# Kernel optimization log

Hardware: AMD Instinct MI355X
Metric: run time of the kernel (lower is better)

The kernel has to match this reference:

```python
import jax, jax.numpy as jnp
import numpy as np

HEADS = 8
EPS = 1e-5


def _quad_sums(a):
    """a: (B,h,H,W,...) -> (B,h,H,W,4,...) sums over the four inclusive
    quadrants [ :h+1,:w+1 | :h+1,w: | h:,:w+1 | h:,w: ] for every (h,w),
    via padded 2D prefix sums over axes (2,3)."""
    c = jnp.cumsum(jnp.cumsum(a, axis=2), axis=3)
    pads = [(0, 0)] * a.ndim
    pads[2] = (1, 0)
    pads[3] = (1, 0)
    P = jnp.pad(c, pads)  # P[...,i,j,...] = sum over rows<i, cols<j
    tl = P[:, :, 1:, 1:]
    tr = P[:, :, 1:, -1:] - P[:, :, 1:, :-1]
    bl = P[:, :, -1:, 1:] - P[:, :, :-1, 1:]
    br = P[:, :, -1:, -1:] - P[:, :, :-1, -1:] - P[:, :, -1:, :-1] + P[:, :, :-1, :-1]
    return jnp.stack([tl, tr, bl, br], axis=4)


def setup_inputs():
    key = jax.random.key(0)
    ks = jax.random.split(key, 12)
    B, H, W, D = 64, 48, 48, 64
    n = H * W
    hD = HEADS * D  # inner_dim = heads * dim_head, dim_head == dim
    rn = lambda k, shape: jax.random.normal(k, shape, dtype=jnp.float32) * 0.02
    return {
        "x": jax.random.normal(ks[0], (B, n, D), dtype=jnp.float32),
        "ln_g": jnp.ones((D,), jnp.float32),
        "ln_b": jnp.zeros((D,), jnp.float32),
        "Wqkv": rn(ks[1], (3 * hD, D)),
        "bqkv": jnp.zeros((3 * hD,), jnp.float32),
        "cls_tok": rn(ks[2], (D,)),
        "Wwqkv": rn(ks[3], (3 * D, D)),
        "bwqkv": jnp.zeros((3 * D,), jnp.float32),
        "Wwproj": rn(ks[4], (D, D)),
        "bwproj": jnp.zeros((D,), jnp.float32),
        "Wraq": rn(ks[5], (D, D)),
        "Wrak": rn(ks[6], (D, D)),
        "Wrav": rn(ks[7], (D, D)),
        "Wrao": rn(ks[8], (D, D)),
        "brao": jnp.zeros((D,), jnp.float32),
        "Wout": rn(ks[9], (D, hD)),
        "bout": jnp.zeros((D,), jnp.float32),
    }


def reference(x, ln_g, ln_b, Wqkv, bqkv, cls_tok, Wwqkv, bwqkv, Wwproj, bwproj,
              Wraq, Wrak, Wrav, Wrao, brao, Wout, bout):
    B, n, D = x.shape
    H = W = int(np.sqrt(n))
    h = HEADS
    hd = D // h                      # WindowAttention head dim
    scale_w = hd ** -0.5             # WindowAttention qk scale
    scale_ra = (D // h) ** -0.5      # RegionAggregator scale

    # LayerNorm (biased variance, as torch)
    mu = x.mean(-1, keepdims=True)
    var = ((x - mu) ** 2).mean(-1, keepdims=True)
    xn = (x - mu) / jnp.sqrt(var + EPS) * ln_g + ln_b

    # to_qkv: only q is consumed downstream (k, v are dead in the original forward)
    q = xn @ Wqkv[: h * D].T + bqkv[: h * D]
    q = q.reshape(B, n, h, D).transpose(0, 2, 1, 3)  # (B,h,n,D)  d == dim

    # WindowAttention: per-quadrant CLS-row attention, shared token keys/values.
    cls_qkv = (cls_tok @ Wwqkv.T + bwqkv).reshape(3, h, hd)
    q_c = cls_qkv[0] * scale_w                       # (h,hd) scaled cls query
    k_c, v_c = cls_qkv[1], cls_qkv[2]
    tok = (xn @ Wwqkv.T + bwqkv).reshape(B, n, 3, h, hd)
    k_t = tok[:, :, 1].transpose(0, 2, 1, 3)         # (B,h,n,hd)
    v_t = tok[:, :, 2].transpose(0, 2, 1, 3)
    logits = jnp.einsum('hd,bhnd->bhn', q_c, k_t)    # cls -> token logits
    cls_logit = jnp.einsum('hd,hd->h', q_c, k_c)     # cls -> cls logit
    m = jnp.maximum(logits.max(-1), cls_logit)       # (B,h) stabilizer
    e = jnp.exp(logits - m[..., None]).reshape(B, h, H, W)
    ecls = jnp.exp(cls_logit - m)                    # (B,h)
    ev = e[..., None] * v_t.reshape(B, h, H, W, hd)
    Se = _quad_sums(e)                               # (B,h,H,W,4)
    Sev = _quad_sums(ev)                             # (B,h,H,W,4,hd)
    denom = ecls[:, :, None, None, None] + Se
    num = ecls[:, :, None, None, None, None] * v_c[None, :, None, None, None, :] + Sev
    cls_out = num / denom[..., None]                 # (B,h,H,W,4,hd)
    cls_out = cls_out.transpose(0, 2, 3, 4, 1, 5).reshape(B, n, 4, D)
    regions = cls_out @ Wwproj.T + bwproj            # (B,n,4,D)

    # RegionAggregator (regions are identical across heads -> broadcast)
    qp = jnp.einsum('bhnd,ed->bhne', q, Wraq)
    kp = regions @ Wrak.T                            # (B,n,4,D)
    vp = regions @ Wrav.T
    scores = jnp.einsum('bhnd,bnrd->bhnr', qp, kp) * scale_ra
    attn = jax.nn.softmax(scores, axis=-1)
    agg = jnp.einsum('bhnr,bnrd->bhnd', attn, vp)
    out = agg @ Wrao.T + brao                        # (B,h,n,D)
    out = out.transpose(0, 2, 1, 3).reshape(B, n, h * D)
    return out @ Wout.T + bout                       # (B,n,D)
```

## Files before the change

kernel.cpp:

```cpp
#include <hip/hip_runtime.h>
#include <math.h>


#define SCALE_W  0.3535533905932738f
#define SCALE_RA 0.3535533905932738f
#define LN_EPS 1e-5f

typedef __attribute__((ext_vector_type(8))) short bf16x8;
typedef __attribute__((ext_vector_type(4))) float f32x4;

#define OFF_XN   0ull
#define SZ_XN    (64ull*2304*64)
#define OFF_KT   (OFF_XN + SZ_XN)
#define SZ_KT    (64ull*8*2304*8)
#define OFF_VT   (OFF_KT + SZ_KT)
#define OFF_PA   (OFF_VT + SZ_KT)
#define SZ_PA    (512ull*2401*5)
#define OFF_PB   (OFF_PA + SZ_PA)
#define SZ_PB    (512ull*2401*4)
#define OFF_ECLS (OFF_PB + SZ_PB)
#define OFF_QC   (OFF_ECLS + 512)
#define OFF_KC   (OFF_QC + 64)
#define OFF_VC   (OFF_KC + 64)
#define OFF_CLOG (OFF_VC + 64)
#define OFF_BK   (OFF_CLOG + 8)
#define OFF_BV   (OFF_BK + 64)
#define OFF_AH   (OFF_BV + 64)
#define OFF_W1   (OFF_AH + 512)
#define OFF_WZ   (OFF_W1 + 64)
#define OFF_B2   (OFF_WZ + 64)
#define OFF_V2   (OFF_B2 + 512)
#define OFF_UH   (OFF_V2 + 512)
#define OFF_CH   (OFF_UH + 512)
#define OFF_C1   (OFF_CH + 8)
#define OFF_G    (OFF_C1 + 64)
#define OFF_Z    (OFF_G + 32768)

__device__ inline void split2(float x, unsigned short &h, unsigned short &l) {
  unsigned u = __float_as_uint(x);
  unsigned hr = (u + 0x7fffu + ((u >> 16) & 1u)) >> 16;
  h = (unsigned short)hr;
  float hf = __uint_as_float(hr << 16);
  float lo = x - hf;
  unsigned u2 = __float_as_uint(lo);
  l = (unsigned short)((u2 + 0x7fffu + ((u2 >> 16) & 1u)) >> 16);
}

__device__ inline void split2x2(float x0, float x1, unsigned &h, unsigned &l) {
  asm("v_cvt_pk_bf16_f32 %0, %1, %2" : "=v"(h) : "v"(x0), "v"(x1));
  float r0 = x0 - __uint_as_float(h << 16);
  float r1 = x1 - __uint_as_float(h & 0xffff0000u);
  asm("v_cvt_pk_bf16_f32 %0, %1, %2" : "=v"(l) : "v"(r0), "v"(r1));
}

__device__ inline float dot64(const float* __restrict__ a, const float* __restrict__ b) {
  float s0 = 0.f, s1 = 0.f, s2 = 0.f, s3 = 0.f;
  #pragma unroll
  for (int d = 0; d < 64; d += 4) {
    float4 av = *(const float4*)(a + d);
    float4 bv = *(const float4*)(b + d);
    s0 += av.x * bv.x; s1 += av.y * bv.y;
    s2 += av.z * bv.z; s3 += av.w * bv.w;
  }
  return (s0 + s1) + (s2 + s3);
}

__global__ void k_setup1(const float* __restrict__ Wqkv, const float* __restrict__ bqkv,
                         const float* __restrict__ cls_tok, const float* __restrict__ Wwqkv,
                         const float* __restrict__ bwqkv, const float* __restrict__ Wwproj,
                         const float* __restrict__ bwproj, const float* __restrict__ Wraq,
                         const float* __restrict__ Wrak, const float* __restrict__ Wrav,
                         const float* __restrict__ Wrao, const float* __restrict__ brao,
                         const float* __restrict__ Wout, const float* __restrict__ bout,
                         float* __restrict__ ws) {
  __shared__ float bwz[64];
  int tid = threadIdx.x;
  for (int idx = tid; idx < 768; idx += 256) {
    if (idx < 192) {
      float s = bwqkv[idx] + dot64(Wwqkv + idx*64, cls_tok);
      if (idx < 64) ws[OFF_QC + idx] = s * SCALE_W;
      else if (idx < 128) ws[OFF_KC + idx - 64] = s;
      else ws[OFF_VC + idx - 128] = s;
    } else if (idx < 256) {
      int e = idx - 192;
      ws[OFF_BV + e] = dot64(Wrav + e*64, bwproj);
    } else {
      int t2 = idx - 256; int hh = t2 >> 6, e = t2 & 63;
      ws[OFF_AH + t2] = dot64(Wraq + e*64, bqkv + hh*64);
    }
  }
  __syncthreads();
  for (int idx = tid; idx < 584; idx += 256) {
    if (idx < 8) {
      float s = 0.f;
      for (int u = 0; u < 8; ++u) s += ws[OFF_QC + idx*8+u] * ws[OFF_KC + idx*8+u];
      ws[OFF_CLOG + idx] = s;
    } else if (idx < 72) {
      int e = idx - 8;
      ws[OFF_WZ + e] = dot64(Wrao + e*64, ws + OFF_BV);
    } else {
      int t2 = idx - 72; int hh = t2 >> 6, e = t2 & 63; float s = 0.f;
      for (int d = 0; d < 64; ++d) s += Wrak[d*64+e] * ws[OFF_AH + hh*64+d];
      ws[OFF_B2 + t2] = s;
    }
  }
  __syncthreads();
  if (tid < 64) bwz[tid] = brao[tid] + ws[OFF_WZ + tid];
  __syncthreads();
  for (int idx = tid; idx < 576; idx += 256) {
    if (idx < 512) {
      int hh = idx >> 6, e = idx & 63; float s = 0.f;
      for (int d = 0; d < 64; ++d) s += Wwproj[d*64+e] * ws[OFF_B2 + hh*64+d];
      ws[OFF_V2 + idx] = s;
    } else {
      int e = idx - 512;
      float s0 = 0.f, s1 = 0.f, s2 = 0.f, s3 = 0.f;
      for (int f = 0; f < 512; f += 4) {
        float4 w4 = *(const float4*)(Wout + e*512 + f);
        float4 b4 = *(const float4*)&bwz[f & 63];
        s0 += w4.x*b4.x; s1 += w4.y*b4.y; s2 += w4.z*b4.z; s3 += w4.w*b4.w;
      }
      ws[OFF_C1 + e] = bout[e] + (s0 + s1) + (s2 + s3);
    }
  }
}

__global__ __launch_bounds__(256) void k_setupW(const float* __restrict__ Wqkv,
      const float* __restrict__ Wraq, const float* __restrict__ Wrak,
      const float* __restrict__ Wrav, const float* __restrict__ Wrao,
      const float* __restrict__ Wwproj, const float* __restrict__ Wout,
      float* __restrict__ ws) {
  __shared__ float A[64*65];
  __shared__ float Bl[64*65];
  int tid = threadIdx.x;
  int blk = blockIdx.x;
  if (blk < 8) {
    int hh = blk;
    for (int o = tid; o < 4096; o += 256) {
      int d = o & 63, e = o >> 6; float s = 0.f;
      for (int f = 0; f < 64; ++f) s += Wraq[f*64+d] * Wrak[f*64+e];
      A[d*65 + e] = s;
    }
    __syncthreads();
    for (int o = tid; o < 4096; o += 256) {
      int j = o & 63, i = o >> 6; float s = 0.f;
      for (int f = 0; f < 64; ++f) s += A[i*65 + f] * Wwproj[f*64 + j];
      Bl[i*65 + j] = s;
    }
    __syncthreads();
    unsigned short* gb = (unsigned short*)(ws + OFF_G) + hh*8192;
    for (int o = tid; o < 4096; o += 256) {
      int d = o & 63, e = o >> 6; float s = 0.f;
      for (int f = 0; f < 64; ++f) s += Wqkv[(hh*64+f)*64 + d] * Bl[f*65 + e];
      unsigned short h16, l16;
      split2(s, h16, l16);
      int base = (e >> 4)*2048 + (d >> 5)*1024 + (((d >> 3) & 3)*16 + (e & 15))*8 + (d & 7);
      gb[base]       = h16;
      gb[base + 512] = l16;
    }
  } else {
    int hh = blk - 8;
    for (int o = tid; o < 4096; o += 256) {
      int d = o & 63, e = o >> 6; float s = 0.f;
      for (int f = 0; f < 64; ++f) s += Wrav[e*64+f] * Wwproj[f*64+d];
      A[e*65 + d] = s;
    }
    __syncthreads();
    for (int o = tid; o < 4096; o += 256) {
      int d = o & 63, i = o >> 6; float s = 0.f;
      for (int f = 0; f < 64; ++f) s += Wrao[i*64+f] * A[f*65 + d];
      Bl[i*65 + d] = s;
    }
    __syncthreads();
    unsigned short* zb = (unsigned short*)(ws + OFF_Z) + hh*8192;
    for (int o = tid; o < 4096; o += 256) {
      int d = o & 63, e = o >> 6; float s = 0.f;
      for (int f = 0; f < 64; ++f) s += Wout[e*512 + hh*64 + f] * Bl[f*65 + d];
      unsigned short h16, l16;
      split2(s, h16, l16);
      int base = (e >> 4)*2048 + (d >> 5)*1024 + (((d >> 3) & 3)*16 + (e & 15))*8 + (d & 7);
      zb[base]       = h16;
      zb[base + 512] = l16;
    }
  }
}

__global__ __launch_bounds__(256) void k_lnkv(const float* __restrict__ x,
      const float* __restrict__ ln_g, const float* __restrict__ ln_b,
      const float* __restrict__ Wwqkv, const float* __restrict__ bwqkv,
      float* __restrict__ ws) {
  __shared__ float sm[4352 + 8448 + 128];
  float* xnT = sm;
  float* xt  = sm + 4352;
  float* wkv = sm + 4352;
  float* muL = sm + 4352 + 8448;
  float* rsL = muL + 64;

  int tid = threadIdx.x;
  long T0 = (long)blockIdx.x * 64;
  int tok = tid >> 2, seg = tid & 3;

  const float4* x4 = (const float4*)(x + (T0 + tok)*64 + seg*16);
  float4 va = x4[0], vb = x4[1], vc4 = x4[2], vd = x4[3];
  {
    float* xp = xt + tok*65 + seg*16;
    xp[0]=va.x; xp[1]=va.y; xp[2]=va.z; xp[3]=va.w;
    xp[4]=vb.x; xp[5]=vb.y; xp[6]=vb.z; xp[7]=vb.w;
    xp[8]=vc4.x; xp[9]=vc4.y; xp[10]=vc4.z; xp[11]=vc4.w;
    xp[12]=vd.x; xp[13]=vd.y; xp[14]=vd.z; xp[15]=vd.w;
  }
  __syncthreads();
  if (tid < 64) {
    float s = 0.f;
    for (int i2 = 0; i2 < 64; ++i2) s += xt[tid*65 + i2];
    float mu = s * (1.0f/64.0f);
    float v = 0.f;
    for (int i2 = 0; i2 < 64; ++i2) { float d = xt[tid*65 + i2] - mu; v += d*d; }
    v *= (1.0f/64.0f);
    muL[tid] = mu; rsL[tid] = 1.0f / sqrtf(v + LN_EPS);
  }
  __syncthreads();
  {
    float mu = muL[tok], rs = rsL[tok];
    float xv[16];
    #pragma unroll
    for (int k = 0; k < 16; ++k) {
      int i2 = seg*16 + k;
      float v = (xt[tok*65 + i2] - mu) * rs * ln_g[i2] + ln_b[i2];
      xv[k] = v;
      xnT[i2*68 + tok] = v;
    }
    float4* xng = (float4*)(ws + OFF_XN + (T0 + tok)*64 + seg*16);
    xng[0] = make_float4(xv[0], xv[1], xv[2], xv[3]);
    xng[1] = make_float4(xv[4], xv[5], xv[6], xv[7]);
    xng[2] = make_float4(xv[8], xv[9], xv[10], xv[11]);
    xng[3] = make_float4(xv[12], xv[13], xv[14], xv[15]);
  }
  __syncthreads();
  {
    int o = tid >> 1, dh = (tid & 1) * 32;
    #pragma unroll
    for (int k = 0; k < 32; k += 4) {
      float4 w4 = *(const float4*)(Wwqkv + (64 + o)*64 + dh + k);
      wkv[(dh+k+0)*132 + o] = w4.x;
      wkv[(dh+k+1)*132 + o] = w4.y;
      wkv[(dh+k+2)*132 + o] = w4.z;
      wkv[(dh+k+3)*132 + o] = w4.w;
    }
  }
  __syncthreads();
  int tokq = tid & 15, og = tid >> 4;
  float acc[4][8];
  #pragma unroll
  for (int ti = 0; ti < 4; ++ti)
    #pragma unroll
    for (int k = 0; k < 8; ++k) acc[ti][k] = 0.f;
  for (int d2 = 0; d2 < 64; ++d2) {
    float4 a4 = *(float4*)&xnT[d2*68 + tokq*4];
    float4 b0 = *(float4*)&wkv[d2*132 + og*8];
    float4 b1 = *(float4*)&wkv[d2*132 + og*8 + 4];
    float aa[4] = {a4.x, a4.y, a4.z, a4.w};
    float bbv[8] = {b0.x,b0.y,b0.z,b0.w,b1.x,b1.y,b1.z,b1.w};
    #pragma unroll
    for (int ti = 0; ti < 4; ++ti)
      #pragma unroll
      for (int k = 0; k < 8; ++k) acc[ti][k] += aa[ti]*bbv[k];
  }
  int hh2 = og & 7;
  float bsv[8];
  #pragma unroll
  for (int k = 0; k < 8; ++k) bsv[k] = bwqkv[64 + og*8 + k];
  unsigned long long dstoff = (og < 8) ? OFF_KT : OFF_VT;
  #pragma unroll
  for (int ti = 0; ti < 4; ++ti) {
    long ntok = T0 + tokq*4 + ti;
    int bb = (int)(ntok / 2304);
    int nl = (int)(ntok % 2304);
    float* dst = ws + dstoff + ((long)(bb*8 + hh2)*2304 + nl)*8;
    *(float4*)dst = make_float4(acc[ti][0]+bsv[0], acc[ti][1]+bsv[1], acc[ti][2]+bsv[2], acc[ti][3]+bsv[3]);
    *(float4*)(dst+4) = make_float4(acc[ti][4]+bsv[4], acc[ti][5]+bsv[5], acc[ti][6]+bsv[6], acc[ti][7]+bsv[7]);
  }
}

__global__ __launch_bounds__(256) void k_prefix(float* __restrict__ ws) {
  __shared__ float Pp[49*49*5];
  __shared__ float red[4];
  int tid = threadIdx.x;
  int blk = blockIdx.x;
  int g = blk & 1, bh = blk >> 1;
  int hh = bh & 7;
  const float* kt = ws + OFF_KT + (long)bh*2304*8;
  const float* vt = ws + OFF_VT + (long)bh*2304*8 + (g ? 4 : 0);
  float qc[8];
  #pragma unroll
  for (int u = 0; u < 8; ++u) qc[u] = ws[OFF_QC + hh*8 + u];
  float lgr[9];
  float mloc = -1e30f;
  #pragma unroll
  for (int it = 0; it < 9; ++it) {
    int nn = tid + it*256;
    const float4* kk = (const float4*)(kt + nn*8);
    float4 k0 = kk[0], k1 = kk[1];
    float lv = qc[0]*k0.x + qc[1]*k0.y + qc[2]*k0.z + qc[3]*k0.w
             + qc[4]*k1.x + qc[5]*k1.y + qc[6]*k1.z + qc[7]*k1.w;
    lgr[it] = lv;
    mloc = fmaxf(mloc, lv);
  }
  #pragma unroll
  for (int mk = 1; mk < 64; mk <<= 1) mloc = fmaxf(mloc, __shfl_xor(mloc, mk, 64));
  if ((tid & 63) == 0) red[tid >> 6] = mloc;
  __syncthreads();
  float m = fmaxf(fmaxf(red[0], red[1]), fmaxf(red[2], red[3]));
  m = fmaxf(m, ws[OFF_CLOG + hh]);
  if (tid == 0 && g == 0) ws[OFF_ECLS + bh] = __expf(ws[OFF_CLOG + hh] - m);
  #pragma unroll
  for (int it = 0; it < 9; ++it) {
    int nn = tid + it*256;
    int i2 = nn / 48, j2 = nn % 48;
    float ev = __expf(lgr[it] - m);
    float4 v4 = *(const float4*)(vt + nn*8);
    float* cell = &Pp[((i2+1)*49 + (j2+1))*5];
    if (g == 0) {
      cell[0] = ev; cell[1] = ev*v4.x; cell[2] = ev*v4.y; cell[3] = ev*v4.z; cell[4] = ev*v4.w;
    } else {
      cell[0] = ev*v4.x; cell[1] = ev*v4.y; cell[2] = ev*v4.z; cell[3] = ev*v4.w;
    }
  }
  __syncthreads();
  int nc = g ? 4 : 5;
  for (int idx = tid; idx < 48*nc; idx += 256) {
    int j2 = idx / nc + 1, c = idx % nc;
    float s = 0.f;
    for (int i0 = 1; i0 <= 48; i0 += 8) {
      float v[8];
      #pragma unroll
      for (int k = 0; k < 8; ++k) v[k] = Pp[((i0+k)*49 + j2)*5 + c];
      #pragma unroll
      for (int k = 0; k < 8; ++k) { s += v[k]; v[k] = s; }
      #pragma unroll
      for (int k = 0; k < 8; ++k) Pp[((i0+k)*49 + j2)*5 + c] = v[k];
    }
  }
  __syncthreads();
  for (int idx = tid; idx < 48*nc; idx += 256) {
    int i2 = idx / nc + 1, c = idx % nc;
    float s = 0.f;
    for (int j0 = 1; j0 <= 48; j0 += 8) {
      float v[8];
      #pragma unroll
      for (int k = 0; k < 8; ++k) v[k] = Pp[(i2*49 + j0+k)*5 + c];
      #pragma unroll
      for (int k = 0; k < 8; ++k) { s += v[k]; v[k] = s; }
      #pragma unroll
      for (int k = 0; k < 8; ++k) Pp[(i2*49 + j0+k)*5 + c] = v[k];
    }
  }
  __syncthreads();
  if (g == 0) {
    float* pa = ws + OFF_PA + (long)bh*12005;
    for (int idx = tid; idx < 12005; idx += 256) {
      int cell = idx / 5;
      int ii = cell / 49, jj = cell % 49;
      pa[idx] = (ii && jj) ? Pp[idx] : 0.f;
    }
  } else {
    float* pb = ws + OFF_PB + (long)bh*9604;
    for (int idx = tid; idx < 9604; idx += 256) {
      int cell = idx >> 2, c = idx & 3;
      int ii = cell / 49, jj = cell % 49;
      pb[idx] = (ii && jj) ? Pp[cell*5 + c] : 0.f;
    }
  }
}

__global__ __launch_bounds__(128) void k_main(const float* __restrict__ ws,
                                              float* __restrict__ outp) {
  __shared__ __align__(16) unsigned short XNhi[16*64];
  __shared__ __align__(16) unsigned short XNlo[16*64];
  __shared__ __align__(16) unsigned short CBhi[16*128];
  __shared__ __align__(16) unsigned short CBlo[16*128];
  __shared__ __align__(16) float Tlds[16*128];

  int tid = threadIdx.x;
  int tok = tid >> 3, eg = tid & 7;
  int lane = tid & 63, wv = tid >> 6;
  int quad = lane >> 4, lrow = lane & 15;
  int wcol = wv;
  long T0 = (long)blockIdx.x * 16;
  int b = (int)(T0 / 2304);
  int n = (int)(T0 % 2304) + tok;
  int i2 = n / 48, j2 = n % 48;

  {
    const float4* p4 = (const float4*)(ws + OFF_XN + (T0 + tok)*64 + eg*8);
    float4 xa = p4[0], xb = p4[1];
    float xv[8] = {xa.x, xa.y, xa.z, xa.w, xb.x, xb.y, xb.z, xb.w};
    union { unsigned u[4]; uint2 d[2]; } ph, pl;
    #pragma unroll
    for (int k = 0; k < 8; k += 2) split2x2(xv[k], xv[k+1], ph.u[k>>1], pl.u[k>>1]);
    int off = tok*64 + ((eg*8) ^ ((tok & 7) << 3));
    *(uint2*)&XNhi[off]     = ph.d[0];
    *(uint2*)&XNhi[off + 4] = ph.d[1];
    *(uint2*)&XNlo[off]     = pl.d[0];
    *(uint2*)&XNlo[off + 4] = pl.d[1];
  }

  float cls0[8], cls1[8], cls2[8], cls3[8];
  {
    float ec = ws[OFF_ECLS + b*8 + eg];
    const float* PA = ws + OFF_PA + (long)(b*8 + eg)*12005;
    const float* PB = ws + OFF_PB + (long)(b*8 + eg)*9604;
    int c_ij  = i2*49 + j2;
    int c_ij1 = c_ij + 1;
    int c_iW  = i2*49 + 48;
    int c_1j  = c_ij + 49;
    int c_1j1 = c_1j + 1;
    int c_1W  = c_iW + 49;
    int c_Hj  = 48*49 + j2;
    int c_Hj1 = c_Hj + 1;
    int c_HW  = 48*49 + 48;
    float rden[4];
    {
      float tl = PA[c_1j1*5];
      float tr = PA[c_1W*5] - PA[c_1j*5];
      float bl = PA[c_Hj1*5] - PA[c_ij1*5];
      float br = PA[c_HW*5] - PA[c_iW*5] - PA[c_Hj*5] + PA[c_ij*5];
      rden[0] = 1.0f/(ec + tl); rden[1] = 1.0f/(ec + tr);
      rden[2] = 1.0f/(ec + bl); rden[3] = 1.0f/(ec + br);
    }
    #pragma unroll
    for (int u = 0; u < 4; ++u) {
      int c = 1 + u;
      float tl = PA[c_1j1*5 + c];
      float tr = PA[c_1W*5 + c] - PA[c_1j*5 + c];
      float bl = PA[c_Hj1*5 + c] - PA[c_ij1*5 + c];
      float br = PA[c_HW*5 + c] - PA[c_iW*5 + c] - PA[c_Hj*5 + c] + PA[c_ij*5 + c];
      float nv = ec * ws[OFF_VC + eg*8 + u];
      cls0[u] = (nv + tl) * rden[0];
      cls1[u] = (nv + tr) * rden[1];
      cls2[u] = (nv + bl) * rden[2];
      cls3[u] = (nv + br) * rden[3];
    }
    #pragma unroll
    for (int u = 4; u < 8; ++u) {
      int c = u - 4;
      float tl = PB[c_1j1*4 + c];
      float tr = PB[c_1W*4 + c] - PB[c_1j*4 + c];
      float bl = PB[c_Hj1*4 + c] - PB[c_ij1*4 + c];
      float br = PB[c_HW*4 + c] - PB[c_iW*4 + c] - PB[c_Hj*4 + c] + PB[c_ij*4 + c];
      float nv = ec * ws[OFF_VC + eg*8 + u];
      cls0[u] = (nv + tl) * rden[0];
      cls1[u] = (nv + tr) * rden[1];
      cls2[u] = (nv + bl) * rden[2];
      cls3[u] = (nv + br) * rden[3];
    }
  }
  __syncthreads();

  const unsigned short* gball = (const unsigned short*)(ws + OFF_G);
  const unsigned short* zball = (const unsigned short*)(ws + OFF_Z);

  f32x4 oa0 = {0.f,0.f,0.f,0.f};
  f32x4 oa1 = {0.f,0.f,0.f,0.f};

  int rr = lrow;
  int sw3 = (rr & 7) << 3;
  const unsigned short* arh = XNhi + rr*64;
  const unsigned short* arl = XNlo + rr*64;
  const unsigned short* crh = CBhi + rr*128;
  const unsigned short* crl = CBlo + rr*128;

  for (int it = 0; it < 4; ++it) {
    int h0 = it*2;
    {
      union { bf16x8 v; uint2 d[2]; } ah0, ah1, al0, al1;
      int oa = (quad*8) ^ sw3;
      int ob = (32 + quad*8) ^ sw3;
      ah0.d[0] = *(const uint2*)(arh + oa); ah0.d[1] = *(const uint2*)(arh + oa + 4);
      ah1.d[0] = *(const uint2*)(arh + ob); ah1.d[1] = *(const uint2*)(arh + ob + 4);
      al0.d[0] = *(const uint2*)(arl + oa); al0.d[1] = *(const uint2*)(arl + oa + 4);
      al1.d[0] = *(const uint2*)(arl + ob); al1.d[1] = *(const uint2*)(arl + ob + 4);
      #pragma unroll
      for (int c = 0; c < 4; ++c) {
        int colb = wcol*4 + c;
        int e0 = colb*16 + lrow;
        const unsigned short* gh = gball + (h0 + (colb >> 2))*8192 + (colb & 3)*2048 + lane*8;
        bf16x8 bh0 = *(const bf16x8*)(gh);
        bf16x8 bl0 = *(const bf16x8*)(gh + 512);
        bf16x8 bh1 = *(const bf16x8*)(gh + 1024);
        bf16x8 bl1 = *(const bf16x8*)(gh + 1536);
        f32x4 acc = {0.f,0.f,0.f,0.f};
        acc = __builtin_amdgcn_mfma_f32_16x16x32_bf16(ah0.v, bh0, acc, 0, 0, 0);
        acc = __builtin_amdgcn_mfma_f32_16x16x32_bf16(ah1.v, bh1, acc, 0, 0, 0);
        acc = __builtin_amdgcn_mfma_f32_16x16x32_bf16(al0.v, bh0, acc, 0, 0, 0);
        acc = __builtin_amdgcn_mfma_f32_16x16x32_bf16(al1.v, bh1, acc, 0, 0, 0);
        acc = __builtin_amdgcn_mfma_f32_16x16x32_bf16(ah0.v, bl0, acc, 0, 0, 0);
        acc = __builtin_amdgcn_mfma_f32_16x16x32_bf16(ah1.v, bl1, acc, 0, 0, 0);
        float v2v = ws[OFF_V2 + h0*64 + e0];
        #pragma unroll
        for (int r = 0; r < 4; ++r) {
          int trow = quad*4 + r;
          Tlds[trow*128 + (e0 ^ ((trow & 7) << 2))] = acc[r] + v2v;
        }
      }
    }
    __syncthreads();
    {
      float tv0[8], tv1[8];
      {
        int base = tok*128;
        int sw2 = (tok & 7) << 2;
        float4 a0 = *(const float4*)&Tlds[base + ((eg*8) ^ sw2)];
        float4 b0 = *(const float4*)&Tlds[base + ((eg*8 + 4) ^ sw2)];
        float4 a1 = *(const float4*)&Tlds[base + ((64 + eg*8) ^ sw2)];
        float4 b1 = *(const float4*)&Tlds[base + ((64 + eg*8 + 4) ^ sw2)];
        tv0[0]=a0.x; tv0[1]=a0.y; tv0[2]=a0.z; tv0[3]=a0.w;
        tv0[4]=b0.x; tv0[5]=b0.y; tv0[6]=b0.z; tv0[7]=b0.w;
        tv1[0]=a1.x; tv1[1]=a1.y; tv1[2]=a1.z; tv1[3]=a1.w;
        tv1[4]=b1.x; tv1[5]=b1.y; tv1[6]=b1.z; tv1[7]=b1.w;
      }
      float p0=0.f,p1=0.f,p2=0.f,p3=0.f,q0=0.f,q1=0.f,q2=0.f,q3=0.f;
      #pragma unroll
      for (int k = 0; k < 8; ++k) {
        p0 += tv0[k]*cls0[k]; p1 += tv0[k]*cls1[k];
        p2 += tv0[k]*cls2[k]; p3 += tv0[k]*cls3[k];
        q0 += tv1[k]*cls0[k]; q1 += tv1[k]*cls1[k];
        q2 += tv1[k]*cls2[k]; q3 += tv1[k]*cls3[k];
      }
      #pragma unroll
      for (int mk = 1; mk < 8; mk <<= 1) {
        p0 += __shfl_xor(p0, mk, 8); p1 += __shfl_xor(p1, mk, 8);
        p2 += __shfl_xor(p2, mk, 8); p3 += __shfl_xor(p3, mk, 8);
        q0 += __shfl_xor(q0, mk, 8); q1 += __shfl_xor(q1, mk, 8);
        q2 += __shfl_xor(q2, mk, 8); q3 += __shfl_xor(q3, mk, 8);
      }
      union { unsigned u[4]; uint2 d[2]; } ch, cl;
      int cbBase = tok*128;
      int swc = (tok & 7) << 3;
      {
        float s0 = p0*SCALE_RA, s1 = p1*SCALE_RA, s2 = p2*SCALE_RA, s3 = p3*SCALE_RA;
        float mm = fmaxf(fmaxf(s0, s1), fmaxf(s2, s3));
        float e0 = __expf(s0-mm), e1 = __expf(s1-mm), e2 = __expf(s2-mm), e3 = __expf(s3-mm);
        float inv = 1.0f/(e0+e1+e2+e3);
        float av0 = e0*inv, av1 = e1*inv, av2 = e2*inv, av3 = e3*inv;
        #pragma unroll
        for (int k = 0; k < 8; k += 2) {
          float cv0 = av0*cls0[k] + av1*cls1[k] + av2*cls2[k] + av3*cls3[k];
          float cv1 = av0*cls0[k+1] + av1*cls1[k+1] + av2*cls2[k+1] + av3*cls3[k+1];
          split2x2(cv0, cv1, ch.u[k>>1], cl.u[k>>1]);
        }
        int o = cbBase + ((eg*8) ^ swc);
        *(uint2*)&CBhi[o]     = ch.d[0]; *(uint2*)&CBhi[o + 4] = ch.d[1];
        *(uint2*)&CBlo[o]     = cl.d[0]; *(uint2*)&CBlo[o + 4] = cl.d[1];
      }
      {
        float s0 = q0*SCALE_RA, s1 = q1*SCALE_RA, s2 = q2*SCALE_RA, s3 = q3*SCALE_RA;
        float mm = fmaxf(fmaxf(s0, s1), fmaxf(s2, s3));
        float e0 = __expf(s0-mm), e1 = __expf(s1-mm), e2 = __expf(s2-mm), e3 = __expf(s3-mm);
        float inv = 1.0f/(e0+e1+e2+e3);
        float av0 = e0*inv, av1 = e1*inv, av2 = e2*inv, av3 = e3*inv;
        #pragma unroll
        for (int k = 0; k < 8; k += 2) {
          float cv0 = av0*cls0[k] + av1*cls1[k] + av2*cls2[k] + av3*cls3[k];
          float cv1 = av0*cls0[k+1] + av1*cls1[k+1] + av2*cls2[k+1] + av3*cls3[k+1];
          split2x2(cv0, cv1, ch.u[k>>1], cl.u[k>>1]);
        }
        int o = cbBase + ((64 + eg*8) ^ swc);
        *(uint2*)&CBhi[o]     = ch.d[0]; *(uint2*)&CBhi[o + 4] = ch.d[1];
        *(uint2*)&CBlo[o]     = cl.d[0]; *(uint2*)&CBlo[o + 4] = cl.d[1];
      }
    }
    __syncthreads();
    {
      #pragma unroll
      for (int c = 0; c < 2; ++c) {
        int colb = wcol*2 + c;
        int e0 = colb*16 + lrow;
        f32x4 acc = (c == 0) ? oa0 : oa1;
        #pragma unroll
        for (int kb = 0; kb < 4; ++kb) {
          union { bf16x8 v; uint2 d[2]; } ah, al;
          int o = (kb*32 + quad*8) ^ sw3;
          ah.d[0] = *(const uint2*)(crh + o); ah.d[1] = *(const uint2*)(crh + o + 4);
          al.d[0] = *(const uint2*)(crl + o); al.d[1] = *(const uint2*)(crl + o + 4);
          const unsigned short* zc = zball + (h0 + (kb >> 1))*8192 + colb*2048 + (kb & 1)*1024 + lane*8;
          bf16x8 bh = *(const bf16x8*)(zc);
          bf16x8 bl = *(const bf16x8*)(zc + 512);
          acc = __builtin_amdgcn_mfma_f32_16x16x32_bf16(ah.v, bh, acc, 0, 0, 0);
          acc = __builtin_amdgcn_mfma_f32_16x16x32_bf16(al.v, bh, acc, 0, 0, 0);
          acc = __builtin_amdgcn_mfma_f32_16x16x32_bf16(ah.v, bl, acc, 0, 0, 0);
        }
        if (c == 0) oa0 = acc; else oa1 = acc;
      }
    }
  }
  #pragma unroll
  for (int c = 0; c < 2; ++c) {
    int e0 = (wcol*2 + c)*16 + lrow;
    float cov = ws[OFF_C1 + e0];
    f32x4 oa = (c == 0) ? oa0 : oa1;
    #pragma unroll
    for (int r = 0; r < 4; ++r)
      outp[(T0 + quad*4 + r)*64 + e0] = oa[r] + cov;
  }
}

extern "C" void kernel_launch(void* const* d_in, const int* in_sizes, int n_in,
                              void* d_out, int out_size, void* d_ws, size_t ws_size,
                              hipStream_t stream) {
  const float* x      = (const float*)d_in[0];
  const float* ln_g   = (const float*)d_in[1];
  const float* ln_b   = (const float*)d_in[2];
  const float* Wqkv   = (const float*)d_in[3];
  const float* bqkv   = (const float*)d_in[4];
  const float* cls_tok= (const float*)d_in[5];
  const float* Wwqkv  = (const float*)d_in[6];
  const float* bwqkv  = (const float*)d_in[7];
  const float* Wwproj = (const float*)d_in[8];
  const float* bwproj = (const float*)d_in[9];
  const float* Wraq   = (const float*)d_in[10];
  const float* Wrak   = (const float*)d_in[11];
  const float* Wrav   = (const float*)d_in[12];
  const float* Wrao   = (const float*)d_in[13];
  const float* brao   = (const float*)d_in[14];
  const float* Wout   = (const float*)d_in[15];
  const float* bout   = (const float*)d_in[16];
  float* ws = (float*)d_ws;
  float* outp = (float*)d_out;

  hipLaunchKernelGGL(k_setup1, dim3(1), dim3(256), 0, stream,
                     Wqkv, bqkv, cls_tok, Wwqkv, bwqkv, Wwproj, bwproj,
                     Wraq, Wrak, Wrav, Wrao, brao, Wout, bout, ws);
  hipLaunchKernelGGL(k_setupW, dim3(16), dim3(256), 0, stream,
                     Wqkv, Wraq, Wrak, Wrav, Wrao, Wwproj, Wout, ws);
  hipLaunchKernelGGL(k_lnkv, dim3(2304), dim3(256), 0, stream, x, ln_g, ln_b, Wwqkv, bwqkv, ws);
  hipLaunchKernelGGL(k_prefix, dim3(1024), dim3(256), 0, stream, ws);
  hipLaunchKernelGGL(k_main, dim3(9216), dim3(128), 0, stream, ws, outp);
}
```

Baseline: 404.7 us.

## Merge setup and layernorm kernels into one launch, widen prefix blocks

Three preprocessing kernels (scalar setup, weight folding, layernorm+KV projection) are merged into a single kernel that picks its role by block index, removing two launches and the serialization between the small setup kernels and the large LN kernel. The prefix-sum kernel moves from 256 to 512 threads, so each thread does fewer tokens and the column/row scans run in one pass. In the main kernel the A-fragment LDS loads are hoisted out of the head loop. The setup blocks now run alongside LN blocks, and their long serial tail can extend the fused kernel.

```diff
diff --git a/kernel.cpp b/kernel.cpp
--- a/kernel.cpp
+++ b/kernel.cpp
@@ -65,226 +65,219 @@
   return (s0 + s1) + (s2 + s3);
 }
 
-__global__ void k_setup1(const float* __restrict__ Wqkv, const float* __restrict__ bqkv,
-                         const float* __restrict__ cls_tok, const float* __restrict__ Wwqkv,
-                         const float* __restrict__ bwqkv, const float* __restrict__ Wwproj,
-                         const float* __restrict__ bwproj, const float* __restrict__ Wraq,
-                         const float* __restrict__ Wrak, const float* __restrict__ Wrav,
-                         const float* __restrict__ Wrao, const float* __restrict__ brao,
-                         const float* __restrict__ Wout, const float* __restrict__ bout,
-                         float* __restrict__ ws) {
-  __shared__ float bwz[64];
-  int tid = threadIdx.x;
-  for (int idx = tid; idx < 768; idx += 256) {
-    if (idx < 192) {
-      float s = bwqkv[idx] + dot64(Wwqkv + idx*64, cls_tok);
-      if (idx < 64) ws[OFF_QC + idx] = s * SCALE_W;
-      else if (idx < 128) ws[OFF_KC + idx - 64] = s;
-      else ws[OFF_VC + idx - 128] = s;
-    } else if (idx < 256) {
-      int e = idx - 192;
-      ws[OFF_BV + e] = dot64(Wrav + e*64, bwproj);
-    } else {
-      int t2 = idx - 256; int hh = t2 >> 6, e = t2 & 63;
-      ws[OFF_AH + t2] = dot64(Wraq + e*64, bqkv + hh*64);
-    }
-  }
-  __syncthreads();
-  for (int idx = tid; idx < 584; idx += 256) {
-    if (idx < 8) {
-      float s = 0.f;
-      for (int u = 0; u < 8; ++u) s += ws[OFF_QC + idx*8+u] * ws[OFF_KC + idx*8+u];
-      ws[OFF_CLOG + idx] = s;
-    } else if (idx < 72) {
-      int e = idx - 8;
-      ws[OFF_WZ + e] = dot64(Wrao + e*64, ws + OFF_BV);
-    } else {
-      int t2 = idx - 72; int hh = t2 >> 6, e = t2 & 63; float s = 0.f;
-      for (int d = 0; d < 64; ++d) s += Wrak[d*64+e] * ws[OFF_AH + hh*64+d];
-      ws[OFF_B2 + t2] = s;
-    }
-  }
-  __syncthreads();
-  if (tid < 64) bwz[tid] = brao[tid] + ws[OFF_WZ + tid];
-  __syncthreads();
-  for (int idx = tid; idx < 576; idx += 256) {
-    if (idx < 512) {
-      int hh = idx >> 6, e = idx & 63; float s = 0.f;
-      for (int d = 0; d < 64; ++d) s += Wwproj[d*64+e] * ws[OFF_B2 + hh*64+d];
-      ws[OFF_V2 + idx] = s;
-    } else {
-      int e = idx - 512;
-      float s0 = 0.f, s1 = 0.f, s2 = 0.f, s3 = 0.f;
-      for (int f = 0; f < 512; f += 4) {
-        float4 w4 = *(const float4*)(Wout + e*512 + f);
-        float4 b4 = *(const float4*)&bwz[f & 63];
-        s0 += w4.x*b4.x; s1 += w4.y*b4.y; s2 += w4.z*b4.z; s3 += w4.w*b4.w;
-      }
-      ws[OFF_C1 + e] = bout[e] + (s0 + s1) + (s2 + s3);
-    }
-  }
-}
-
-__global__ __launch_bounds__(256) void k_setupW(const float* __restrict__ Wqkv,
-      const float* __restrict__ Wraq, const float* __restrict__ Wrak,
-      const float* __restrict__ Wrav, const float* __restrict__ Wrao,
-      const float* __restrict__ Wwproj, const float* __restrict__ Wout,
+__global__ __launch_bounds__(256) void k_pre(const float* __restrict__ x,
+      const float* __restrict__ ln_g, const float* __restrict__ ln_b,
+      const float* __restrict__ Wqkv, const float* __restrict__ bqkv,
+      const float* __restrict__ cls_tok, const float* __restrict__ Wwqkv,
+      const float* __restrict__ bwqkv, const float* __restrict__ Wwproj,
+      const float* __restrict__ bwproj, const float* __restrict__ Wraq,
+      const float* __restrict__ Wrak, const float* __restrict__ Wrav,
+      const float* __restrict__ Wrao, const float* __restrict__ brao,
+      const float* __restrict__ Wout, const float* __restrict__ bout,
       float* __restrict__ ws) {
-  __shared__ float A[64*65];
-  __shared__ float Bl[64*65];
+  __shared__ float smu[12928];
   int tid = threadIdx.x;
   int blk = blockIdx.x;
-  if (blk < 8) {
-    int hh = blk;
-    for (int o = tid; o < 4096; o += 256) {
-      int d = o & 63, e = o >> 6; float s = 0.f;
-      for (int f = 0; f < 64; ++f) s += Wraq[f*64+d] * Wrak[f*64+e];
-      A[d*65 + e] = s;
-    }
-    __syncthreads();
-    for (int o = tid; o < 4096; o += 256) {
-      int j = o & 63, i = o >> 6; float s = 0.f;
-      for (int f = 0; f < 64; ++f) s += A[i*65 + f] * Wwproj[f*64 + j];
-      Bl[i*65 + j] = s;
-    }
-    __syncthreads();
-    unsigned short* gb = (unsigned short*)(ws + OFF_G) + hh*8192;
-    for (int o = tid; o < 4096; o += 256) {
-      int d = o & 63, e = o >> 6; float s = 0.f;
-      for (int f = 0; f < 64; ++f) s += Wqkv[(hh*64+f)*64 + d] * Bl[f*65 + e];
-      unsigned short h16, l16;
-      split2(s, h16, l16);
-      int base = (e >> 4)*2048 + (d >> 5)*1024 + (((d >> 3) & 3)*16 + (e & 15))*8 + (d & 7);
-      gb[base]       = h16;
-      gb[base + 512] = l16;
-    }
-  } else {
-    int hh = blk - 8;
-    for (int o = tid; o < 4096; o += 256) {
-      int d = o & 63, e = o >> 6; float s = 0.f;
-      for (int f = 0; f < 64; ++f) s += Wrav[e*64+f] * Wwproj[f*64+d];
-      A[e*65 + d] = s;
-    }
-    __syncthreads();
-    for (int o = tid; o < 4096; o += 256) {
-      int d = o & 63, i = o >> 6; float s = 0.f;
-      for (int f = 0; f < 64; ++f) s += Wrao[i*64+f] * A[f*65 + d];
-      Bl[i*65 + d] = s;
-    }
-    __syncthreads();
-    unsigned short* zb = (unsigned short*)(ws + OFF_Z) + hh*8192;
-    for (int o = tid; o < 4096; o += 256) {
-      int d = o & 63, e = o >> 6; float s = 0.f;
-      for (int f = 0; f < 64; ++f) s += Wout[e*512 + hh*64 + f] * Bl[f*65 + d];
-      unsigned short h16, l16;
-      split2(s, h16, l16);
-      int base = (e >> 4)*2048 + (d >> 5)*1024 + (((d >> 3) & 3)*16 + (e & 15))*8 + (d & 7);
-      zb[base]       = h16;
-      zb[base + 512] = l16;
-    }
-  }
-}
-
-__global__ __launch_bounds__(256) void k_lnkv(const float* __restrict__ x,
-      const float* __restrict__ ln_g, const float* __restrict__ ln_b,
-      const float* __restrict__ Wwqkv, const float* __restrict__ bwqkv,
-      float* __restrict__ ws) {
-  __shared__ float sm[4352 + 8448 + 128];
-  float* xnT = sm;
-  float* xt  = sm + 4352;
-  float* wkv = sm + 4352;
-  float* muL = sm + 4352 + 8448;
-  float* rsL = muL + 64;
-
-  int tid = threadIdx.x;
-  long T0 = (long)blockIdx.x * 64;
-  int tok = tid >> 2, seg = tid & 3;
-
-  const float4* x4 = (const float4*)(x + (T0 + tok)*64 + seg*16);
-  float4 va = x4[0], vb = x4[1], vc4 = x4[2], vd = x4[3];
-  {
-    float* xp = xt + tok*65 + seg*16;
-    xp[0]=va.x; xp[1]=va.y; xp[2]=va.z; xp[3]=va.w;
-    xp[4]=vb.x; xp[5]=vb.y; xp[6]=vb.z; xp[7]=vb.w;
-    xp[8]=vc4.x; xp[9]=vc4.y; xp[10]=vc4.z; xp[11]=vc4.w;
-    xp[12]=vd.x; xp[13]=vd.y; xp[14]=vd.z; xp[15]=vd.w;
-  }
-  __syncthreads();
-  if (tid < 64) {
-    float s = 0.f;
-    for (int i2 = 0; i2 < 64; ++i2) s += xt[tid*65 + i2];
-    float mu = s * (1.0f/64.0f);
-    float v = 0.f;
-    for (int i2 = 0; i2 < 64; ++i2) { float d = xt[tid*65 + i2] - mu; v += d*d; }
-    v *= (1.0f/64.0f);
-    muL[tid] = mu; rsL[tid] = 1.0f / sqrtf(v + LN_EPS);
-  }
-  __syncthreads();
-  {
-    float mu = muL[tok], rs = rsL[tok];
-    float xv[16];
-    #pragma unroll
-    for (int k = 0; k < 16; ++k) {
-      int i2 = seg*16 + k;
-      float v = (xt[tok*65 + i2] - mu) * rs * ln_g[i2] + ln_b[i2];
-      xv[k] = v;
-      xnT[i2*68 + tok] = v;
-    }
-    float4* xng = (float4*)(ws + OFF_XN + (T0 + tok)*64 + seg*16);
-    xng[0] = make_float4(xv[0], xv[1], xv[2], xv[3]);
-    xng[1] = make_float4(xv[4], xv[5], xv[6], xv[7]);
-    xng[2] = make_float4(xv[8], xv[9], xv[10], xv[11]);
-    xng[3] = make_float4(xv[12], xv[13], xv[14], xv[15]);
-  }
-  __syncthreads();
-  {
-    int o = tid >> 1, dh = (tid & 1) * 32;
-    #pragma unroll
-    for (int k = 0; k < 32; k += 4) {
-      float4 w4 = *(const float4*)(Wwqkv + (64 + o)*64 + dh + k);
-      wkv[(dh+k+0)*132 + o] = w4.x;
-      wkv[(dh+k+1)*132 + o] = w4.y;
-      wkv[(dh+k+2)*132 + o] = w4.z;
-      wkv[(dh+k+3)*132 + o] = w4.w;
-    }
-  }
-  __syncthreads();
-  int tokq = tid & 15, og = tid >> 4;
-  float acc[4][8];
-  #pragma unroll
-  for (int ti = 0; ti < 4; ++ti)
-    #pragma unroll
-    for (int k = 0; k < 8; ++k) acc[ti][k] = 0.f;
-  for (int d2 = 0; d2 < 64; ++d2) {
-    float4 a4 = *(float4*)&xnT[d2*68 + tokq*4];
-    float4 b0 = *(float4*)&wkv[d2*132 + og*8];
-    float4 b1 = *(float4*)&wkv[d2*132 + og*8 + 4];
-    float aa[4] = {a4.x, a4.y, a4.z, a4.w};
-    float bbv[8] = {b0.x,b0.y,b0.z,b0.w,b1.x,b1.y,b1.z,b1.w};
+
+  if (blk < 2304) {
+    float* xnT = smu;
+    float* xt  = smu + 4352;
+    float* wkv = smu + 4352;
+    float* muL = smu + 4352 + 8448;
+    float* rsL = muL + 64;
+
+    long T0 = (long)blk * 64;
+    int tok = tid >> 2, seg = tid & 3;
+
+    const float4* x4 = (const float4*)(x + (T0 + tok)*64 + seg*16);
+    float4 va = x4[0], vb = x4[1], vc4 = x4[2], vd = x4[3];
+    {
+      float* xp = xt + tok*65 + seg*16;
+      xp[0]=va.x; xp[1]=va.y; xp[2]=va.z; xp[3]=va.w;
+      xp[4]=vb.x; xp[5]=vb.y; xp[6]=vb.z; xp[7]=vb.w;
+      xp[8]=vc4.x; xp[9]=vc4.y; xp[10]=vc4.z; xp[11]=vc4.w;
+      xp[12]=vd.x; xp[13]=vd.y; xp[14]=vd.z; xp[15]=vd.w;
+    }
+    __syncthreads();
+    if (tid < 64) {
+      float s = 0.f;
+      for (int i2 = 0; i2 < 64; ++i2) s += xt[tid*65 + i2];
+      float mu = s * (1.0f/64.0f);
+      float v = 0.f;
+      for (int i2 = 0; i2 < 64; ++i2) { float d = xt[tid*65 + i2] - mu; v += d*d; }
+      v *= (1.0f/64.0f);
+      muL[tid] = mu; rsL[tid] = 1.0f / sqrtf(v + LN_EPS);
+    }
+    __syncthreads();
+    {
+      float mu = muL[tok], rs = rsL[tok];
+      float xv[16];
+      #pragma unroll
+      for (int k = 0; k < 16; ++k) {
+        int i2 = seg*16 + k;
+        float v = (xt[tok*65 + i2] - mu) * rs * ln_g[i2] + ln_b[i2];
+        xv[k] = v;
+        xnT[i2*68 + tok] = v;
+      }
+      float4* xng = (float4*)(ws + OFF_XN + (T0 + tok)*64 + seg*16);
+      xng[0] = make_float4(xv[0], xv[1], xv[2], xv[3]);
+      xng[1] = make_float4(xv[4], xv[5], xv[6], xv[7]);
+      xng[2] = make_float4(xv[8], xv[9], xv[10], xv[11]);
+      xng[3] = make_float4(xv[12], xv[13], xv[14], xv[15]);
+    }
+    __syncthreads();
+    {
+      int o = tid >> 1, dh = (tid & 1) * 32;
+      #pragma unroll
+      for (int k = 0; k < 32; k += 4) {
+        float4 w4 = *(const float4*)(Wwqkv + (64 + o)*64 + dh + k);
+        wkv[(dh+k+0)*132 + o] = w4.x;
+        wkv[(dh+k+1)*132 + o] = w4.y;
+        wkv[(dh+k+2)*132 + o] = w4.z;
+        wkv[(dh+k+3)*132 + o] = w4.w;
+      }
+    }
+    __syncthreads();
+    int tokq = tid & 15, og = tid >> 4;
+    float acc[4][8];
     #pragma unroll
     for (int ti = 0; ti < 4; ++ti)
       #pragma unroll
-      for (int k = 0; k < 8; ++k) acc[ti][k] += aa[ti]*bbv[k];
-  }
-  int hh2 = og & 7;
-  float bsv[8];
-  #pragma unroll
-  for (int k = 0; k < 8; ++k) bsv[k] = bwqkv[64 + og*8 + k];
-  unsigned long long dstoff = (og < 8) ? OFF_KT : OFF_VT;
-  #pragma unroll
-  for (int ti = 0; ti < 4; ++ti) {
-    long ntok = T0 + tokq*4 + ti;
-    int bb = (int)(ntok / 2304);
-    int nl = (int)(ntok % 2304);
-    float* dst = ws + dstoff + ((long)(bb*8 + hh2)*2304 + nl)*8;
-    *(float4*)dst = make_float4(acc[ti][0]+bsv[0], acc[ti][1]+bsv[1], acc[ti][2]+bsv[2], acc[ti][3]+bsv[3]);
-    *(float4*)(dst+4) = make_float4(acc[ti][4]+bsv[4], acc[ti][5]+bsv[5], acc[ti][6]+bsv[6], acc[ti][7]+bsv[7]);
+      for (int k = 0; k < 8; ++k) acc[ti][k] = 0.f;
+    for (int d2 = 0; d2 < 64; ++d2) {
+      float4 a4 = *(float4*)&xnT[d2*68 + tokq*4];
+      float4 b0 = *(float4*)&wkv[d2*132 + og*8];
+      float4 b1 = *(float4*)&wkv[d2*132 + og*8 + 4];
+      float aa[4] = {a4.x, a4.y, a4.z, a4.w};
+      float bbv[8] = {b0.x,b0.y,b0.z,b0.w,b1.x,b1.y,b1.z,b1.w};
+      #pragma unroll
+      for (int ti = 0; ti < 4; ++ti)
+        #pragma unroll
+        for (int k = 0; k < 8; ++k) acc[ti][k] += aa[ti]*bbv[k];
+    }
+    int hh2 = og & 7;
+    float bsv[8];
+    #pragma unroll
+    for (int k = 0; k < 8; ++k) bsv[k] = bwqkv[64 + og*8 + k];
+    unsigned long long dstoff = (og < 8) ? OFF_KT : OFF_VT;
+    #pragma unroll
+    for (int ti = 0; ti < 4; ++ti) {
+      long ntok = T0 + tokq*4 + ti;
+      int bb = (int)(ntok / 2304);
+      int nl = (int)(ntok % 2304);
+      float* dst = ws + dstoff + ((long)(bb*8 + hh2)*2304 + nl)*8;
+      *(float4*)dst = make_float4(acc[ti][0]+bsv[0], acc[ti][1]+bsv[1], acc[ti][2]+bsv[2], acc[ti][3]+bsv[3]);
+      *(float4*)(dst+4) = make_float4(acc[ti][4]+bsv[4], acc[ti][5]+bsv[5], acc[ti][6]+bsv[6], acc[ti][7]+bsv[7]);
+    }
+  } else if (blk < 2320) {
+    float* A  = smu;
+    float* Bl = smu + 4160;
+    int wblk = blk - 2304;
+    if (wblk < 8) {
+      int hh = wblk;
+      for (int o = tid; o < 4096; o += 256) {
+        int d = o & 63, e = o >> 6; float s = 0.f;
+        for (int f = 0; f < 64; ++f) s += Wraq[f*64+d] * Wrak[f*64+e];
+        A[d*65 + e] = s;
+      }
+      __syncthreads();
+      for (int o = tid; o < 4096; o += 256) {
+        int j = o & 63, i = o >> 6; float s = 0.f;
+        for (int f = 0; f < 64; ++f) s += A[i*65 + f] * Wwproj[f*64 + j];
+        Bl[i*65 + j] = s;
+      }
+      __syncthreads();
+      unsigned short* gb = (unsigned short*)(ws + OFF_G) + hh*8192;
+      for (int o = tid; o < 4096; o += 256) {
+        int d = o & 63, e = o >> 6; float s = 0.f;
+        for (int f = 0; f < 64; ++f) s += Wqkv[(hh*64+f)*64 + d] * Bl[f*65 + e];
+        unsigned short h16, l16;
+        split2(s, h16, l16);
+        int base = (e >> 4)*2048 + (d >> 5)*1024 + (((d >> 3) & 3)*16 + (e & 15))*8 + (d & 7);
+        gb[base]       = h16;
+        gb[base + 512] = l16;
+      }
+    } else {
+      int hh = wblk - 8;
+      for (int o = tid; o < 4096; o += 256) {
+        int d = o & 63, e = o >> 6; float s = 0.f;
+        for (int f = 0; f < 64; ++f) s += Wrav[e*64+f] * Wwproj[f*64+d];
+        A[e*65 + d] = s;
+      }
+      __syncthreads();
+      for (int o = tid; o < 4096; o += 256) {
+        int d = o & 63, i = o >> 6; float s = 0.f;
+        for (int f = 0; f < 64; ++f) s += Wrao[i*64+f] * A[f*65 + d];
+        Bl[i*65 + d] = s;
+      }
+      __syncthreads();
+      unsigned short* zb = (unsigned short*)(ws + OFF_Z) + hh*8192;
+      for (int o = tid; o < 4096; o += 256) {
+        int d = o & 63, e = o >> 6; float s = 0.f;
+        for (int f = 0; f < 64; ++f) s += Wout[e*512 + hh*64 + f] * Bl[f*65 + d];
+        unsigned short h16, l16;
+        split2(s, h16, l16);
+        int base = (e >> 4)*2048 + (d >> 5)*1024 + (((d >> 3) & 3)*16 + (e & 15))*8 + (d & 7);
+        zb[base]       = h16;
+        zb[base + 512] = l16;
+      }
+    }
+  } else {
+    float* bwz = smu;
+    for (int idx = tid; idx < 768; idx += 256) {
+      if (idx < 192) {
+        float s = bwqkv[idx] + dot64(Wwqkv + idx*64, cls_tok);
+        if (idx < 64) ws[OFF_QC + idx] = s * SCALE_W;
+        else if (idx < 128) ws[OFF_KC + idx - 64] = s;
+        else ws[OFF_VC + idx - 128] = s;
+      } else if (idx < 256) {
+        int e = idx - 192;
+        ws[OFF_BV + e] = dot64(Wrav + e*64, bwproj);
+      } else {
+        int t2 = idx - 256; int hh = t2 >> 6, e = t2 & 63;
+        ws[OFF_AH + t2] = dot64(Wraq + e*64, bqkv + hh*64);
+      }
+    }
+    __syncthreads();
+    for (int idx = tid; idx < 584; idx += 256) {
+      if (idx < 8) {
+        float s = 0.f;
+        for (int u = 0; u < 8; ++u) s += ws[OFF_QC + idx*8+u] * ws[OFF_KC + idx*8+u];
+        ws[OFF_CLOG + idx] = s;
+      } else if (idx < 72) {
+        int e = idx - 8;
+        ws[OFF_WZ + e] = dot64(Wrao + e*64, ws + OFF_BV);
+      } else {
+        int t2 = idx - 72; int hh = t2 >> 6, e = t2 & 63; float s = 0.f;
+        for (int d = 0; d < 64; ++d) s += Wrak[d*64+e] * ws[OFF_AH + hh*64+d];
+        ws[OFF_B2 + t2] = s;
+      }
+    }
+    __syncthreads();
+    if (tid < 64) bwz[tid] = brao[tid] + ws[OFF_WZ + tid];
+    __syncthreads();
+    for (int idx = tid; idx < 576; idx += 256) {
+      if (idx < 512) {
+        int hh = idx >> 6, e = idx & 63; float s = 0.f;
+        for (int d = 0; d < 64; ++d) s += Wwproj[d*64+e] * ws[OFF_B2 + hh*64+d];
+        ws[OFF_V2 + idx] = s;
+      } else {
+        int e = idx - 512;
+        float s0 = 0.f, s1 = 0.f, s2 = 0.f, s3 = 0.f;
+        for (int f = 0; f < 512; f += 4) {
+          float4 w4 = *(const float4*)(Wout + e*512 + f);
+          float4 b4 = *(const float4*)&bwz[f & 63];
+          s0 += w4.x*b4.x; s1 += w4.y*b4.y; s2 += w4.z*b4.z; s3 += w4.w*b4.w;
+        }
+        ws[OFF_C1 + e] = bout[e] + (s0 + s1) + (s2 + s3);
+      }
+    }
   }
 }
 
-__global__ __launch_bounds__(256) void k_prefix(float* __restrict__ ws) {
+__global__ __launch_bounds__(512) void k_prefix(float* __restrict__ ws) {
   __shared__ float Pp[49*49*5];
-  __shared__ float red[4];
+  __shared__ float red[8];
   int tid = threadIdx.x;
   int blk = blockIdx.x;
   int g = blk & 1, bh = blk >> 1;
@@ -294,42 +287,47 @@
   float qc[8];
   #pragma unroll
   for (int u = 0; u < 8; ++u) qc[u] = ws[OFF_QC + hh*8 + u];
-  float lgr[9];
+  float lgr[5];
   float mloc = -1e30f;
   #pragma unroll
-  for (int it = 0; it < 9; ++it) {
-    int nn = tid + it*256;
-    const float4* kk = (const float4*)(kt + nn*8);
-    float4 k0 = kk[0], k1 = kk[1];
-    float lv = qc[0]*k0.x + qc[1]*k0.y + qc[2]*k0.z + qc[3]*k0.w
-             + qc[4]*k1.x + qc[5]*k1.y + qc[6]*k1.z + qc[7]*k1.w;
-    lgr[it] = lv;
-    mloc = fmaxf(mloc, lv);
+  for (int it = 0; it < 5; ++it) {
+    int nn = tid + it*512;
+    if (nn < 2304) {
+      const float4* kk = (const float4*)(kt + nn*8);
+      float4 k0 = kk[0], k1 = kk[1];
+      float lv = qc[0]*k0.x + qc[1]*k0.y + qc[2]*k0.z + qc[3]*k0.w
+               + qc[4]*k1.x + qc[5]*k1.y + qc[6]*k1.z + qc[7]*k1.w;
+      lgr[it] = lv;
+      mloc = fmaxf(mloc, lv);
+    }
   }
   #pragma unroll
   for (int mk = 1; mk < 64; mk <<= 1) mloc = fmaxf(mloc, __shfl_xor(mloc, mk, 64));
   if ((tid & 63) == 0) red[tid >> 6] = mloc;
   __syncthreads();
-  float m = fmaxf(fmaxf(red[0], red[1]), fmaxf(red[2], red[3]));
+  float m = fmaxf(fmaxf(fmaxf(red[0], red[1]), fmaxf(red[2], red[3])),
+                  fmaxf(fmaxf(red[4], red[5]), fmaxf(red[6], red[7])));
   m = fmaxf(m, ws[OFF_CLOG + hh]);
   if (tid == 0 && g == 0) ws[OFF_ECLS + bh] = __expf(ws[OFF_CLOG + hh] - m);
   #pragma unroll
-  for (int it = 0; it < 9; ++it) {
-    int nn = tid + it*256;
-    int i2 = nn / 48, j2 = nn % 48;
-    float ev = __expf(lgr[it] - m);
-    float4 v4 = *(const float4*)(vt + nn*8);
-    float* cell = &Pp[((i2+1)*49 + (j2+1))*5];
-    if (g == 0) {
-      cell[0] = ev; cell[1] = ev*v4.x; cell[2] = ev*v4.y; cell[3] = ev*v4.z; cell[4] = ev*v4.w;
-    } else {
-      cell[0] = ev*v4.x; cell[1] = ev*v4.y; cell[2] = ev*v4.z; cell[3] = ev*v4.w;
+  for (int it = 0; it < 5; ++it) {
+    int nn = tid + it*512;
+    if (nn < 2304) {
+      int i2 = nn / 48, j2 = nn % 48;
+      float ev = __expf(lgr[it] - m);
+      float4 v4 = *(const float4*)(vt + nn*8);
+      float* cell = &Pp[((i2+1)*49 + (j2+1))*5];
+      if (g == 0) {
+        cell[0] = ev; cell[1] = ev*v4.x; cell[2] = ev*v4.y; cell[3] = ev*v4.z; cell[4] = ev*v4.w;
+      } else {
+        cell[0] = ev*v4.x; cell[1] = ev*v4.y; cell[2] = ev*v4.z; cell[3] = ev*v4.w;
+      }
     }
   }
   __syncthreads();
   int nc = g ? 4 : 5;
-  for (int idx = tid; idx < 48*nc; idx += 256) {
-    int j2 = idx / nc + 1, c = idx % nc;
+  if (tid < 48*nc) {
+    int j2 = tid / nc + 1, c = tid % nc;
     float s = 0.f;
     for (int i0 = 1; i0 <= 48; i0 += 8) {
       float v[8];
@@ -342,8 +340,8 @@
     }
   }
   __syncthreads();
-  for (int idx = tid; idx < 48*nc; idx += 256) {
-    int i2 = idx / nc + 1, c = idx % nc;
+  if (tid < 48*nc) {
+    int i2 = tid / nc + 1, c = tid % nc;
     float s = 0.f;
     for (int j0 = 1; j0 <= 48; j0 += 8) {
       float v[8];
@@ -358,14 +356,14 @@
   __syncthreads();
   if (g == 0) {
     float* pa = ws + OFF_PA + (long)bh*12005;
-    for (int idx = tid; idx < 12005; idx += 256) {
+    for (int idx = tid; idx < 12005; idx += 512) {
       int cell = idx / 5;
       int ii = cell / 49, jj = cell % 49;
       pa[idx] = (ii && jj) ? Pp[idx] : 0.f;
     }
   } else {
     float* pb = ws + OFF_PB + (long)bh*9604;
-    for (int idx = tid; idx < 9604; idx += 256) {
+    for (int idx = tid; idx < 9604; idx += 512) {
       int cell = idx >> 2, c = idx & 3;
       int ii = cell / 49, jj = cell % 49;
       pb[idx] = (ii && jj) ? Pp[cell*5 + c] : 0.f;
@@ -470,16 +468,19 @@
   const unsigned short* crh = CBhi + rr*128;
   const unsigned short* crl = CBlo + rr*128;
 
+  union { bf16x8 v; uint2 d[2]; } ah0, ah1, al0, al1;
+  {
+    int oaa = (quad*8) ^ sw3;
+    int obb = (32 + quad*8) ^ sw3;
+    ah0.d[0] = *(const uint2*)(arh + oaa); ah0.d[1] = *(const uint2*)(arh + oaa + 4);
+    ah1.d[0] = *(const uint2*)(arh + obb); ah1.d[1] = *(const uint2*)(arh + obb + 4);
+    al0.d[0] = *(const uint2*)(arl + oaa); al0.d[1] = *(const uint2*)(arl + oaa + 4);
+    al1.d[0] = *(const uint2*)(arl + obb); al1.d[1] = *(const uint2*)(arl + obb + 4);
+  }
+
   for (int it = 0; it < 4; ++it) {
     int h0 = it*2;
     {
-      union { bf16x8 v; uint2 d[2]; } ah0, ah1, al0, al1;
-      int oa = (quad*8) ^ sw3;
-      int ob = (32 + quad*8) ^ sw3;
-      ah0.d[0] = *(const uint2*)(arh + oa); ah0.d[1] = *(const uint2*)(arh + oa + 4);
-      ah1.d[0] = *(const uint2*)(arh + ob); ah1.d[1] = *(const uint2*)(arh + ob + 4);
-      al0.d[0] = *(const uint2*)(arl + oa); al0.d[1] = *(const uint2*)(arl + oa + 4);
-      al1.d[0] = *(const uint2*)(arl + ob); al1.d[1] = *(const uint2*)(arl + ob + 4);
       #pragma unroll
       for (int c = 0; c < 4; ++c) {
         int colb = wcol*4 + c;
@@ -628,12 +629,9 @@
   float* ws = (float*)d_ws;
   float* outp = (float*)d_out;
 
-  hipLaunchKernelGGL(k_setup1, dim3(1), dim3(256), 0, stream,
-                     Wqkv, bqkv, cls_tok, Wwqkv, bwqkv, Wwproj, bwproj,
-                     Wraq, Wrak, Wrav, Wrao, brao, Wout, bout, ws);
-  hipLaunchKernelGGL(k_setupW, dim3(16), dim3(256), 0, stream,
-                     Wqkv, Wraq, Wrak, Wrav, Wrao, Wwproj, Wout, ws);
-  hipLaunchKernelGGL(k_lnkv, dim3(2304), dim3(256), 0, stream, x, ln_g, ln_b, Wwqkv, bwqkv, ws);
-  hipLaunchKernelGGL(k_prefix, dim3(1024), dim3(256), 0, stream, ws);
+  hipLaunchKernelGGL(k_pre, dim3(2321), dim3(256), 0, stream,
+                     x, ln_g, ln_b, Wqkv, bqkv, cls_tok, Wwqkv, bwqkv,
+                     Wwproj, bwproj, Wraq, Wrak, Wrav, Wrao, brao, Wout, bout, ws);
+  hipLaunchKernelGGL(k_prefix, dim3(1024), dim3(512), 0, stream, ws);
   hipLaunchKernelGGL(k_main, dim3(9216), dim3(128), 0, stream, ws, outp);
 }
```

Result: no change. 411.8 us (+1.8%).
